# Kernel optimization log

Hardware: AMD Instinct MI355X
Metric: run time of the kernel (lower is better)

## Reference

```python
import jax, jax.numpy as jnp
import numpy as np

SIGMA = 0.05
KSIZE = 3
MIN_VAL = 50.0
MAX_VAL = 100.0


def _gauss_kernel():
    # ax = range(-(3//2)+1, 3//2+1) = [-1, 0, 1]  (matches TF int-floor-div)
    ax = jnp.arange(-(KSIZE // 2) + 1.0, KSIZE // 2 + 1.0)
    xx, yy = jnp.meshgrid(ax, ax)
    k = jnp.exp(-(xx ** 2 + yy ** 2) / (2.0 * SIGMA ** 2))
    k = k / jnp.sum(k)
    return k[..., None, None].astype(jnp.float32)  # HWIO, C=1


def _reflect_pad(x):
    return jnp.pad(x, ((0, 0), (1, 1), (1, 1), (0, 0)), mode='reflect')


def _conv(x, k):
    return jax.lax.conv_general_dilated(x, k, (1, 1), 'VALID',
                                        dimension_numbers=('NHWC', 'HWIO', 'NHWC'))


def _canny(images):
    blur = _conv(_reflect_pad(images), _gauss_kernel())
    h = jnp.array([[-1, 0, 1], [-2, 0, 2], [-1, 0, 1]], jnp.float32)[..., None, None]
    v = jnp.array([[-1, -2, -1], [0, 0, 0], [1, 2, 1]], jnp.float32)[..., None, None]
    bp = _reflect_pad(blur)
    gx = _conv(bp, h)
    gy = _conv(bp, v)
    gxy = jnp.sqrt(gx ** 2 + gy ** 2)
    # NOTE: original uses atan2(gx, gy) in this arg order
    theta = (jnp.arctan2(gx, gy) * (180.0 / np.pi) + 90.0) % 180.0

    H, W = gx.shape[1], gx.shape[2]
    # dilation2d with a -inf/0 kernel == max over the kernel's zero-offsets of the
    # zero-padded image; offsets are (dy,dx) of the 0 entries of each 3x3 filter.
    offsets = [
        [(1, 0), (1, 1), (1, 2)],  # horizontal bin: middle row
        [(0, 2), (1, 1), (2, 0)],  # 45 deg: anti-diagonal
        [(0, 1), (1, 1), (2, 1)],  # vertical bin: middle column
        [(0, 0), (1, 1), (2, 2)],  # 135 deg: main diagonal
    ]
    conds = [
        jnp.logical_or(theta >= 157.5, theta < 22.5),
        jnp.logical_and(theta >= 22.5, theta < 67.5),
        jnp.logical_and(theta >= 67.5, theta < 112.5),
        jnp.logical_and(theta >= 112.5, theta < 157.5),
    ]

    edge = jnp.zeros_like(gxy)
    for cond, offs in zip(conds, offsets):
        ang = jnp.where(cond, gxy, 0.0)
        pad = jnp.pad(ang, ((0, 0), (1, 1), (1, 1), (0, 0)))  # zero pad, as ZeroPadding2D
        mp = pad[:, offs[0][0]:offs[0][0] + H, offs[0][1]:offs[0][1] + W, :]
        for dy, dx in offs[1:]:
            mp = jnp.maximum(mp, pad[:, dy:dy + H, dx:dx + W, :])
        edge = edge + jnp.where(mp == ang, ang, 0.0)

    edge_sure = jnp.where(edge >= MAX_VAL, 255.0, 0.0)
    edge_week = jnp.where(jnp.logical_and(edge >= MIN_VAL, edge < MAX_VAL), 255.0, 0.0)
    edge_image = jnp.where(jnp.logical_or(edge_week == 255.0, edge_sure == 255.0), 255.5, 0.0)
    return edge_image, edge_week, edge_sure


def setup_inputs() -> dict:
    key = jax.random.key(0)
    images = jax.random.uniform(key, (16, 1024, 1024, 1), dtype=jnp.float32) * 255.0
    return {"images": images}


def reference(images):
    return _canny(images)
```

## Files before the change

kernel.cpp:

```cpp
#include <hip/hip_runtime.h>
#include <math.h>

#define IMG_H 1024
#define IMG_W 1024
#define OUT_H 1025
#define OUT_W 1025
#define NIMG  16
#define TOTAL (NIMG * OUT_H * OUT_W)

#define TILE_W 64
#define TILE_H 16
#define HALO_W (TILE_W + 2)
#define HALO_H (TILE_H + 2)
#define NHALO  (HALO_W * HALO_H)

__device__ __forceinline__ int refl(int k) {
    if (k >= 2) return (k <= 1025) ? (k - 2) : 1022;
    return k;
}

__device__ __forceinline__ void sobel(const float* __restrict__ img, int i, int j,
                                      float& gx, float& gy) {
    int r0 = refl(i), r1 = refl(i + 1), r2 = refl(i + 2);
    int c0 = refl(j), c1 = refl(j + 1), c2 = refl(j + 2);
    const float* p0 = img + r0 * IMG_W;
    const float* p1 = img + r1 * IMG_W;
    const float* p2 = img + r2 * IMG_W;
    float v00 = p0[c0], v01 = p0[c1], v02 = p0[c2];
    float v10 = p1[c0],               v12 = p1[c2];
    float v20 = p2[c0], v21 = p2[c1], v22 = p2[c2];

    float t = -v00;
    t = __fadd_rn(t, v02);
    t = __fadd_rn(t, -2.0f * v10);
    t = __fadd_rn(t, 2.0f * v12);
    t = __fadd_rn(t, -v20);
    gx = __fadd_rn(t, v22);

    t = -v00;
    t = __fadd_rn(t, -2.0f * v01);
    t = __fadd_rn(t, -v02);
    t = __fadd_rn(t, v20);
    t = __fadd_rn(t, 2.0f * v21);
    gy = __fadd_rn(t, v22);
}

__device__ int classify_slow(float gx, float gy) {
    float t = (float)atan2((double)gx, (double)gy);
    float deg = __fmul_rn(t, (float)(180.0 / M_PI));
    float th = __fadd_rn(deg, 90.0f);
    th = fmodf(th, 180.0f);
    if (th < 0.0f) th += 180.0f;
    if (th < 22.5f || th >= 157.5f) return 0;
    if (th < 67.5f) return 1;
    if (th < 112.5f) return 2;
    return 3;
}

__device__ __forceinline__ int classify(float gx, float gy) {
    float ax = fabsf(gx), ay = fabsf(gy);
    const float T22_LO = 0.414172141e0f;
    const float T22_HI = 0.414254984e0f;
    const float T67_LO = 2.413972141e0f;
    const float T67_HI = 2.414454984e0f;

    if (ax <= ay * T22_LO) return 2;
    if (ax >= ay * T67_HI) return 0;
    if (ax >= ay * T22_HI && ax <= ay * T67_LO) {
        unsigned s = (__float_as_uint(gx) ^ __float_as_uint(gy)) >> 31;
        return s ? 1 : 3;
    }
    return classify_slow(gx, gy);
}

__device__ __forceinline__ float mag(float gx, float gy) {
    return __fsqrt_rn(__fadd_rn(__fmul_rn(gx, gx), __fmul_rn(gy, gy)));
}

__global__ __launch_bounds__(256) void canny_kernel(const float* __restrict__ images,
                                                    float* __restrict__ out) {
    __shared__ float         g_s[NHALO];
    __shared__ unsigned char b_s[NHALO];

    const int tile_ox = blockIdx.x * TILE_W;
    const int tile_oy = blockIdx.y * TILE_H;
    const int n       = blockIdx.z;
    const float* img = images + (size_t)n * IMG_H * IMG_W;
    const int t = threadIdx.x;

    for (int idx = t; idx < NHALO; idx += 256) {
        int hy = idx / HALO_W;
        int hx = idx - hy * HALO_W;
        int oy = tile_oy + hy - 1;
        int ox = tile_ox + hx - 1;
        float g = -1.0f;
        int   b = 255;
        if (oy >= 0 && oy < OUT_H && ox >= 0 && ox < OUT_W) {
            float gx, gy;
            sobel(img, oy, ox, gx, gy);
            g = mag(gx, gy);
            b = classify(gx, gy);
        }
        g_s[idx] = g;
        b_s[idx] = (unsigned char)b;
    }
    __syncthreads();

    const int col = t & (TILE_W - 1);
    const int row0 = t >> 6;
    const int ox = tile_ox + col;
    if (ox >= OUT_W) return;

    #pragma unroll
    for (int q = 0; q < 4; q++) {
        int r = row0 + q * 4;
        int oy = tile_oy + r;
        if (oy >= OUT_H) continue;

        int hc = (r + 1) * HALO_W + (col + 1);
        float gc = g_s[hc];
        int   bc = b_s[hc];

        int doff;
        switch (bc) {
            case 0:  doff = 1;            break;
            case 1:  doff = HALO_W - 1;   break;
            case 2:  doff = HALO_W;       break;
            default: doff = HALO_W + 1;   break;
        }

        float nmax = 0.0f;
        float g1 = g_s[hc + doff];
        if (b_s[hc + doff] == bc && g1 > nmax) nmax = g1;
        float g2 = g_s[hc - doff];
        if (b_s[hc - doff] == bc && g2 > nmax) nmax = g2;

        float e = (gc >= nmax) ? gc : 0.0f;

        size_t o = (size_t)(n * OUT_H + oy) * OUT_W + ox;
        out[o]                       = (e >= 50.0f) ? 255.5f : 0.0f;
        out[(size_t)TOTAL + o]       = (e >= 50.0f && e < 100.0f) ? 255.0f : 0.0f;
        out[(size_t)(2 * TOTAL) + o] = (e >= 100.0f) ? 255.0f : 0.0f;
    }
}

extern "C" void kernel_launch(void* const* d_in, const int* in_sizes, int n_in,
                              void* d_out, int out_size, void* d_ws, size_t ws_size,
                              hipStream_t stream) {
    const float* images = (const float*)d_in[0];
    float* out = (float*)d_out;
    dim3 grid((OUT_W + TILE_W - 1) / TILE_W,
              (OUT_H + TILE_H - 1) / TILE_H,
              NIMG);
    canny_kernel<<<grid, 256, 0, stream>>>(images, out);
}
```

Measured before the change: 315.5 us.

## Compute Sobel in 4-wide quads with vector loads and packed bin bytes

Each thread in the halo phase now computes gradient magnitude and direction bin for four adjacent pixels. It loads three 6-float rows with float4/float2 vector loads and reuses them across the quad, instead of doing nine scalar loads per pixel. Results go to shared memory as float4 stores plus one packed 32-bit word of bins. The block grows to 320 threads so the whole halo is covered in one pass. This aims to cut redundant global loads and per-pixel index arithmetic, at the cost of a separate generic path for border quads and a less regular output mapping in the second phase.

```diff
diff --git a/kernel.cpp b/kernel.cpp
--- a/kernel.cpp
+++ b/kernel.cpp
@@ -10,17 +10,19 @@
 
 #define TILE_W 64
 #define TILE_H 16
-#define HALO_W (TILE_W + 2)
-#define HALO_H (TILE_H + 2)
-#define NHALO  (HALO_W * HALO_H)
+#define HALO_W 68
+#define HALO_H 18
+#define NQX    17
+#define NQUAD  (HALO_H * NQX)
+#define NTHREADS 320
 
 __device__ __forceinline__ int refl(int k) {
     if (k >= 2) return (k <= 1025) ? (k - 2) : 1022;
     return k;
 }
 
-__device__ __forceinline__ void sobel(const float* __restrict__ img, int i, int j,
-                                      float& gx, float& gy) {
+__device__ __forceinline__ void sobel_generic(const float* __restrict__ img, int i, int j,
+                                              float& gx, float& gy) {
     int r0 = refl(i), r1 = refl(i + 1), r2 = refl(i + 2);
     int c0 = refl(j), c1 = refl(j + 1), c2 = refl(j + 2);
     const float* p0 = img + r0 * IMG_W;
@@ -77,10 +79,16 @@
     return __fsqrt_rn(__fadd_rn(__fmul_rn(gx, gx), __fmul_rn(gy, gy)));
 }
 
-__global__ __launch_bounds__(256) void canny_kernel(const float* __restrict__ images,
-                                                    float* __restrict__ out) {
-    __shared__ float         g_s[NHALO];
-    __shared__ unsigned char b_s[NHALO];
+__device__ __forceinline__ void load6(const float* __restrict__ p, float v[6]) {
+    float4 a = *(const float4*)p;
+    float2 b = *(const float2*)(p + 4);
+    v[0] = a.x; v[1] = a.y; v[2] = a.z; v[3] = a.w; v[4] = b.x; v[5] = b.y;
+}
+
+__global__ __launch_bounds__(NTHREADS) void canny_kernel(const float* __restrict__ images,
+                                                         float* __restrict__ out) {
+    __shared__ float    g_s[HALO_H * HALO_W];
+    __shared__ unsigned b_u[HALO_H * NQX];
 
     const int tile_ox = blockIdx.x * TILE_W;
     const int tile_oy = blockIdx.y * TILE_H;
@@ -88,46 +96,84 @@
     const float* img = images + (size_t)n * IMG_H * IMG_W;
     const int t = threadIdx.x;
 
-    for (int idx = t; idx < NHALO; idx += 256) {
-        int hy = idx / HALO_W;
-        int hx = idx - hy * HALO_W;
-        int oy = tile_oy + hy - 1;
-        int ox = tile_ox + hx - 1;
-        float g = -1.0f;
-        int   b = 255;
-        if (oy >= 0 && oy < OUT_H && ox >= 0 && ox < OUT_W) {
-            float gx, gy;
-            sobel(img, oy, ox, gx, gy);
-            g = mag(gx, gy);
-            b = classify(gx, gy);
+    if (t < NQUAD) {
+        int hy  = t / NQX;
+        int qx  = t - hy * NQX;
+        int oy  = tile_oy + hy - 1;
+        int ox0 = tile_ox + qx * 4 - 2;
+
+        float    gq[4];
+        unsigned bq[4];
+
+        if (oy >= 2 && oy <= 1023 && ox0 >= 2 && ox0 <= 1020) {
+            const float* r0p = img + (oy - 2) * IMG_W + (ox0 - 2);
+            float R0[6], R1[6], R2[6];
+            load6(r0p, R0);
+            load6(r0p + IMG_W, R1);
+            load6(r0p + 2 * IMG_W, R2);
+            #pragma unroll
+            for (int p = 0; p < 4; p++) {
+                float v00 = R0[p], v01 = R0[p + 1], v02 = R0[p + 2];
+                float v10 = R1[p],                  v12 = R1[p + 2];
+                float v20 = R2[p], v21 = R2[p + 1], v22 = R2[p + 2];
+
+                float s = -v00;
+                s = __fadd_rn(s, v02);
+                s = __fadd_rn(s, -2.0f * v10);
+                s = __fadd_rn(s, 2.0f * v12);
+                s = __fadd_rn(s, -v20);
+                float gx = __fadd_rn(s, v22);
+
+                s = -v00;
+                s = __fadd_rn(s, -2.0f * v01);
+                s = __fadd_rn(s, -v02);
+                s = __fadd_rn(s, v20);
+                s = __fadd_rn(s, 2.0f * v21);
+                float gy = __fadd_rn(s, v22);
+
+                gq[p] = mag(gx, gy);
+                bq[p] = (unsigned)classify(gx, gy);
+            }
+        } else {
+            #pragma unroll
+            for (int p = 0; p < 4; p++) {
+                int ox = ox0 + p;
+                float g = -1.0f;
+                unsigned b = 255u;
+                if (oy >= 0 && oy < OUT_H && ox >= 0 && ox < OUT_W) {
+                    float gx, gy;
+                    sobel_generic(img, oy, ox, gx, gy);
+                    g = mag(gx, gy);
+                    b = (unsigned)classify(gx, gy);
+                }
+                gq[p] = g;
+                bq[p] = b;
+            }
         }
-        g_s[idx] = g;
-        b_s[idx] = (unsigned char)b;
+
+        int ldoff = hy * HALO_W + qx * 4;
+        *(float4*)&g_s[ldoff] = make_float4(gq[0], gq[1], gq[2], gq[3]);
+        b_u[hy * NQX + qx] = bq[0] | (bq[1] << 8) | (bq[2] << 16) | (bq[3] << 24);
     }
     __syncthreads();
 
-    const int col = t & (TILE_W - 1);
-    const int row0 = t >> 6;
-    const int ox = tile_ox + col;
-    if (ox >= OUT_W) return;
-
+    const unsigned char* b_s = (const unsigned char*)b_u;
     #pragma unroll
     for (int q = 0; q < 4; q++) {
-        int r = row0 + q * 4;
-        int oy = tile_oy + r;
-        if (oy >= OUT_H) continue;
-
-        int hc = (r + 1) * HALO_W + (col + 1);
+        int p = t + NTHREADS * q;
+        if (p >= TILE_W * TILE_H) break;
+        int r = p >> 6, c = p & 63;
+        int oy = tile_oy + r, ox = tile_ox + c;
+        if (oy >= OUT_H || ox >= OUT_W) continue;
+
+        int hc = (r + 1) * HALO_W + (c + 2);
         float gc = g_s[hc];
         int   bc = b_s[hc];
 
-        int doff;
-        switch (bc) {
-            case 0:  doff = 1;            break;
-            case 1:  doff = HALO_W - 1;   break;
-            case 2:  doff = HALO_W;       break;
-            default: doff = HALO_W + 1;   break;
-        }
+        int doff = (bc == 0) ? 1
+                 : (bc == 1) ? (HALO_W - 1)
+                 : (bc == 2) ? HALO_W
+                 :             (HALO_W + 1);
 
         float nmax = 0.0f;
         float g1 = g_s[hc + doff];
@@ -152,5 +198,5 @@
     dim3 grid((OUT_W + TILE_W - 1) / TILE_W,
               (OUT_H + TILE_H - 1) / TILE_H,
               NIMG);
-    canny_kernel<<<grid, 256, 0, stream>>>(images, out);
-}
+    canny_kernel<<<grid, NTHREADS, 0, stream>>>(images, out);
+}
```

Measured after the change: 297.8 us. 1.06x faster.
